# Performance work log

Hardware: AMD Instinct MI355X
Metric: run time of the kernel (lower is better)

The kernel has to match this reference:

```python
import jax, jax.numpy as jnp
import numpy as np

N_EXPERTS = 8
TOP_K = 2
HIDDEN = 768
INTER = 2048

def setup_inputs() -> dict:
    key = jax.random.key(0)
    ks = jax.random.split(key, 12)
    s_in = 1.0 / np.sqrt(HIDDEN)
    s_mid = 1.0 / np.sqrt(INTER)
    return {
        "x": jax.random.normal(ks[0], (4, 64, 64, HIDDEN), dtype=jnp.float32),
        # gate: nn.Parameter(randn(E, d))
        "gate_w": jax.random.normal(ks[1], (N_EXPERTS, HIDDEN), dtype=jnp.float32),
        # routed experts, stacked: fc1 (d->f), fc2 (f->d)
        "fc1_w": jax.random.uniform(ks[2], (N_EXPERTS, INTER, HIDDEN), jnp.float32, -s_in, s_in),
        "fc1_b": jax.random.uniform(ks[3], (N_EXPERTS, INTER), jnp.float32, -s_in, s_in),
        "fc2_w": jax.random.uniform(ks[4], (N_EXPERTS, HIDDEN, INTER), jnp.float32, -s_mid, s_mid),
        "fc2_b": jax.random.uniform(ks[5], (N_EXPERTS, HIDDEN), jnp.float32, -s_mid, s_mid),
        # shared MLP (gated): w1 (d->f), w3 (d->f), w2 (f->d)
        "w1_w": jax.random.uniform(ks[6], (INTER, HIDDEN), jnp.float32, -s_in, s_in),
        "w1_b": jax.random.uniform(ks[7], (INTER,), jnp.float32, -s_in, s_in),
        "w3_w": jax.random.uniform(ks[8], (INTER, HIDDEN), jnp.float32, -s_in, s_in),
        "w3_b": jax.random.uniform(ks[9], (INTER,), jnp.float32, -s_in, s_in),
        "w2_w": jax.random.uniform(ks[10], (HIDDEN, INTER), jnp.float32, -s_mid, s_mid),
        "w2_b": jax.random.uniform(ks[11], (HIDDEN,), jnp.float32, -s_mid, s_mid),
    }

def _gelu(h):
    # torch nn.GELU / F.gelu default = exact (erf) form
    return jax.nn.gelu(h, approximate=False)

def reference(x, gate_w, fc1_w, fc1_b, fc2_w, fc2_b,
              w1_w, w1_b, w3_w, w3_b, w2_w, w2_b):
    B, H, W, C = x.shape
    xf = x.reshape(-1, C)                                  # [T, d]
    # gate: softmax over experts, top-k, renormalize
    scores = jax.nn.softmax(xf @ gate_w.T, axis=-1)        # [T, E]
    top_v, top_i = jax.lax.top_k(scores, TOP_K)            # [T, k]
    top_v = top_v / jnp.sum(top_v, axis=-1, keepdims=True)
    # routed experts: dense-mask combine (weight 0 => zero contribution,
    # same math as gather-GEMM-scatter without data-dependent shapes)
    out = jnp.zeros_like(xf)
    for e in range(N_EXPERTS):
        w_e = jnp.sum(jnp.where(top_i == e, top_v, 0.0), axis=-1)   # [T]
        h = _gelu(xf @ fc1_w[e].T + fc1_b[e])                        # [T, f]
        y = h @ fc2_w[e].T + fc2_b[e]                                # [T, d]
        out = out + w_e[:, None] * y
    # shared gated MLP
    shared = (_gelu(xf @ w1_w.T + w1_b) * (xf @ w3_w.T + w3_b)) @ w2_w.T + w2_b
    return (out + shared).reshape(B, H, W, C)
```

## Files before the change

### kernel.cpp

```cpp
#include <hip/hip_runtime.h>
#include <math.h>

#define T_TOK 16384
#define DH 768
#define DF 2048
#define NE 8
#define NSLOT (2 * T_TOK)
#define MT_ROUTED 264
#define NROW_H (MT_ROUTED * 128)

typedef __attribute__((ext_vector_type(8))) short bf16x8;
typedef __attribute__((ext_vector_type(4))) float f32x4;

__device__ __forceinline__ unsigned short f2bf(float f) {
  union { float f; unsigned int u; } v; v.f = f;
  unsigned int u = v.u;
  u += 0x7fffu + ((u >> 16) & 1u);
  return (unsigned short)(u >> 16);
}
__device__ __forceinline__ float bf2f(unsigned short s) {
  union { unsigned int u; float f; } v; v.u = ((unsigned int)s) << 16; return v.f;
}

__device__ __forceinline__ float gelu_exact(float x) {
  return 0.5f * x * (1.0f + erff(x * 0.70710678118654752440f));
}

__device__ __forceinline__ unsigned short* yrow(unsigned short* ylo,
                                                unsigned short* yhi, int s) {
  return (s < T_TOK) ? (ylo + (long)s * DH) : (yhi + (long)(s - T_TOK) * DH);
}

__device__ __forceinline__ void async_cp16(void* lds, const void* g) {
  __builtin_amdgcn_global_load_lds(
      (const __attribute__((address_space(1))) unsigned int*)(unsigned long long)g,
      (__attribute__((address_space(3))) unsigned int*)(unsigned int)(unsigned long long)lds,
      16, 0, 0);
}

__global__ __launch_bounds__(256) void conv_f32_bf16(
    const float* __restrict__ src, unsigned short* __restrict__ dst, int n4) {
  int i = blockIdx.x * blockDim.x + threadIdx.x;
  if (i >= n4) return;
  const float4 v = ((const float4*)src)[i];
  union { unsigned short us[4]; unsigned long long u64; } o;
  o.us[0] = f2bf(v.x); o.us[1] = f2bf(v.y); o.us[2] = f2bf(v.z); o.us[3] = f2bf(v.w);
  ((unsigned long long*)dst)[i] = o.u64;
}

__global__ __launch_bounds__(256) void gate_topk(
    const float* __restrict__ x, const float* __restrict__ gw,
    unsigned short* __restrict__ xb, int* __restrict__ eids,
    float* __restrict__ wts) {
  const int wave = threadIdx.x >> 6;
  const int lane = threadIdx.x & 63;
  const int t = blockIdx.x * 4 + wave;
  float4 xv[3];
#pragma unroll
  for (int i = 0; i < 3; ++i) {
    const int c = i * 256 + lane * 4;
    xv[i] = *(const float4*)&x[(long)t * DH + c];
    ushort4 o;
    o.x = f2bf(xv[i].x); o.y = f2bf(xv[i].y);
    o.z = f2bf(xv[i].z); o.w = f2bf(xv[i].w);
    *(ushort4*)&xb[(long)t * DH + c] = o;
  }
  float s[NE];
#pragma unroll
  for (int e = 0; e < NE; ++e) {
    float a = 0.f;
#pragma unroll
    for (int i = 0; i < 3; ++i) {
      const float4 g = *(const float4*)&gw[e * DH + i * 256 + lane * 4];
      a += xv[i].x * g.x + xv[i].y * g.y + xv[i].z * g.z + xv[i].w * g.w;
    }
    s[e] = a;
  }
#pragma unroll
  for (int off = 32; off >= 1; off >>= 1) {
#pragma unroll
    for (int e = 0; e < NE; ++e) s[e] += __shfl_xor(s[e], off);
  }
  if (lane == 0) {
    float b1 = s[0]; int i1 = 0;
#pragma unroll
    for (int e = 1; e < NE; ++e) { if (s[e] > b1) { b1 = s[e]; i1 = e; } }
    float b2 = -3.4e38f; int i2 = 0;
#pragma unroll
    for (int e = 0; e < NE; ++e) {
      if (e != i1 && s[e] > b2) { b2 = s[e]; i2 = e; }
    }
    const float ex = expf(b2 - b1);
    eids[2 * t]     = i1; wts[2 * t]     = 1.f / (1.f + ex);
    eids[2 * t + 1] = i2; wts[2 * t + 1] = ex / (1.f + ex);
  }
}

__global__ __launch_bounds__(256) void hist_k(
    const int* __restrict__ eids, int* __restrict__ hcur) {
  const int j = blockIdx.x * 256 + threadIdx.x;
  const int lane = threadIdx.x & 63;
  const int eid = eids[j];
#pragma unroll
  for (int e = 0; e < NE; ++e) {
    const unsigned long long m = __ballot(eid == e);
    const int tot = __popcll(m);
    if (tot && lane == (__ffsll((long long)m) - 1)) atomicAdd(&hcur[e * 64], tot);
  }
}

__global__ void scan_k(const int* __restrict__ hcur, int* __restrict__ sched,
                       int* __restrict__ cur2) {
  if (threadIdx.x == 0) {
    int b = 0;
#pragma unroll
    for (int e = 0; e < NE; ++e) {
      const int c = hcur[e * 64];
      sched[e] = b; sched[9 + e] = c; cur2[e * 64] = b;
      b += (c + 127) & ~127;
    }
    sched[8] = b;
  }
}

__global__ __launch_bounds__(256) void scatter_k(
    const int* __restrict__ eids, const float* __restrict__ wts,
    int* __restrict__ cur2, int* __restrict__ slot_tok,
    float* __restrict__ slot_wt, int* __restrict__ slot_pos) {
  const int j = blockIdx.x * 256 + threadIdx.x;
  const int lane = threadIdx.x & 63;
  const int eid = eids[j];
  const float w = wts[j];
#pragma unroll
  for (int e = 0; e < NE; ++e) {
    const unsigned long long m = __ballot(eid == e);
    const int tot = __popcll(m);
    if (!tot) continue;
    const int leader = __ffsll((long long)m) - 1;
    int b = 0;
    if (lane == leader) b = atomicAdd(&cur2[e * 64], tot);
    b = __shfl(b, leader);
    if (eid == e) {
      const int pos = b + __popcll(m & ((1ull << lane) - 1));
      slot_tok[pos] = j;
      slot_wt[pos] = w;
      slot_pos[j] = pos;
    }
  }
}

template <int MODE, int GX, int GTOT>
__global__ __launch_bounds__(256, 2) void gemm_k(
    const unsigned short* __restrict__ A, const unsigned short* __restrict__ B1,
    const unsigned short* __restrict__ B2, const float* __restrict__ bias1,
    const float* __restrict__ bias2, float* __restrict__ outF,
    unsigned short* __restrict__ outH, int K,
    const int* __restrict__ sched, const int* __restrict__ slot_tok,
    const int* __restrict__ slot_pos, const float* __restrict__ wts,
    unsigned short* __restrict__ ylo, unsigned short* __restrict__ yhi) {
  constexpr int BPX = (GTOT + 7) / 8;
  const int id = blockIdx.x;
  const int yx = (id & 7) * BPX + (id >> 3);
  const int n0 = (yx % GX) * 128;
  const int m0 = (yx / GX) * 128;

  const int tid = threadIdx.x;
  const int wave = tid >> 6;
  const int lane = tid & 63;
  const int wm = wave >> 1, wn = wave & 1;
  const int l16 = lane & 15, quad = lane >> 4;

  const unsigned short* Bbase = B1;
  const float* bias = bias1;
  int cnt_end = 0;
  if constexpr (MODE == 1 || MODE == 3 || MODE == 4) {
    if (m0 >= sched[8]) return;
    int e = 0;
#pragma unroll
    for (int i = 1; i < NE; ++i) { if (m0 >= sched[i]) e = i; }
    cnt_end = sched[e] + sched[9 + e];
    Bbase = B1 + (long)e * ((long)DF * DH);
    bias = bias1 + e * ((MODE == 1) ? DF : DH);
  }

  __shared__ __align__(16) unsigned short As[128 * 32];
  __shared__ __align__(16) unsigned short Bs[128 * 32];
  __shared__ __align__(16) unsigned short Cs[(MODE == 0) ? 128 * 32 : 16];

  const int srow0 = wave * 16 + (lane >> 2);
  const int srow1 = 64 + srow0;
  const int scol = (lane & 3) * 8;

  long ar0, ar1;
  if constexpr (MODE == 1) {
    const int p0 = m0 + srow0, p1 = m0 + srow1;
    const int t0 = (p0 < cnt_end) ? (slot_tok[p0] >> 1) : 0;
    const int t1 = (p1 < cnt_end) ? (slot_tok[p1] >> 1) : 0;
    ar0 = (long)t0 * K; ar1 = (long)t1 * K;
  } else {
    ar0 = (long)(m0 + srow0) * K;
    ar1 = (long)(m0 + srow1) * K;
  }
  const unsigned short* ap0 = A + ar0 + scol;
  const unsigned short* ap1 = A + ar1 + scol;
  const unsigned short* bp0 = Bbase + (long)(n0 + srow0) * K + scol;
  const unsigned short* bp1 = Bbase + (long)(n0 + srow1) * K + scol;
  const unsigned short* cp0 = nullptr; const unsigned short* cp1 = nullptr;
  if constexpr (MODE == 0) {
    cp0 = B2 + (long)(n0 + srow0) * K + scol;
    cp1 = B2 + (long)(n0 + srow1) * K + scol;
  }

  unsigned short* AsW = &As[wave * 512];
  unsigned short* BsW = &Bs[wave * 512];
  unsigned short* CsW = nullptr;
  if constexpr (MODE == 0) CsW = &Cs[wave * 512];

  f32x4 acc[4][4];
  f32x4 acc2[(MODE == 0) ? 4 : 1][(MODE == 0) ? 4 : 1];
#pragma unroll
  for (int i = 0; i < 4; ++i) {
#pragma unroll
    for (int j = 0; j < 4; ++j) {
      acc[i][j] = {0.f, 0.f, 0.f, 0.f};
      if constexpr (MODE == 0) acc2[i][j] = {0.f, 0.f, 0.f, 0.f};
    }
  }

  const int KT = K >> 5;
  for (int kt = 0; kt < KT; ++kt) {
    const int ko = kt << 5;
    async_cp16(AsW,        ap0 + ko);
    async_cp16(AsW + 2048, ap1 + ko);
    async_cp16(BsW,        bp0 + ko);
    async_cp16(BsW + 2048, bp1 + ko);
    if constexpr (MODE == 0) {
      async_cp16(CsW,        cp0 + ko);
      async_cp16(CsW + 2048, cp1 + ko);
    }
    __syncthreads();

    bf16x8 af[4], bfr[4], cfr[(MODE == 0) ? 4 : 1];
#pragma unroll
    for (int mi = 0; mi < 4; ++mi)
      af[mi] = *(const bf16x8*)&As[(wm * 64 + mi * 16 + l16) * 32 + quad * 8];
#pragma unroll
    for (int ni = 0; ni < 4; ++ni) {
      bfr[ni] = *(const bf16x8*)&Bs[(wn * 64 + ni * 16 + l16) * 32 + quad * 8];
      if constexpr (MODE == 0)
        cfr[ni] = *(const bf16x8*)&Cs[(wn * 64 + ni * 16 + l16) * 32 + quad * 8];
    }
#pragma unroll
    for (int mi = 0; mi < 4; ++mi) {
#pragma unroll
      for (int ni = 0; ni < 4; ++ni) {
        acc[mi][ni] = __builtin_amdgcn_mfma_f32_16x16x32_bf16(
            af[mi], bfr[ni], acc[mi][ni], 0, 0, 0);
        if constexpr (MODE == 0)
          acc2[mi][ni] = __builtin_amdgcn_mfma_f32_16x16x32_bf16(
              af[mi], cfr[ni], acc2[mi][ni], 0, 0, 0);
      }
    }
    __syncthreads();
  }

#pragma unroll
  for (int mi = 0; mi < 4; ++mi) {
#pragma unroll
    for (int r = 0; r < 4; ++r) {
      const int row = m0 + wm * 64 + mi * 16 + quad * 4 + r;
      if constexpr (MODE == 3) {
        unsigned short* yr = yrow(ylo, yhi, row);
#pragma unroll
        for (int ni = 0; ni < 4; ++ni) {
          const int c = n0 + wn * 64 + ni * 16 + l16;
          yr[c] = f2bf(acc[mi][ni][r] + bias[c]);
        }
      } else if constexpr (MODE == 4) {
        if (row < cnt_end) {
          const int t = slot_tok[row] >> 1;
          const float w = wts[row];
#pragma unroll
          for (int ni = 0; ni < 4; ++ni) {
            const int c = n0 + wn * 64 + ni * 16 + l16;
            atomicAdd(&outF[(long)t * DH + c], w * (acc[mi][ni][r] + bias[c]));
          }
        }
      } else if constexpr (MODE == 2) {
        const int s0 = slot_pos[2 * row], s1 = slot_pos[2 * row + 1];
        const float w0 = wts[2 * row], w1 = wts[2 * row + 1];
        const unsigned short* y0 = yrow(ylo, yhi, s0);
        const unsigned short* y1 = yrow(ylo, yhi, s1);
#pragma unroll
        for (int ni = 0; ni < 4; ++ni) {
          const int c = n0 + wn * 64 + ni * 16 + l16;
          outF[(long)row * DH + c] =
              acc[mi][ni][r] + bias[c] + w0 * bf2f(y0[c]) + w1 * bf2f(y1[c]);
        }
      } else if constexpr (MODE == 5) {
#pragma unroll
        for (int ni = 0; ni < 4; ++ni) {
          const int c = n0 + wn * 64 + ni * 16 + l16;
          outF[(long)row * DH + c] = acc[mi][ni][r] + bias[c];
        }
      } else if constexpr (MODE == 1) {
#pragma unroll
        for (int ni = 0; ni < 4; ++ni) {
          const int c = n0 + wn * 64 + ni * 16 + l16;
          outH[(long)row * DF + c] = f2bf(gelu_exact(acc[mi][ni][r] + bias[c]));
        }
      } else {
#pragma unroll
        for (int ni = 0; ni < 4; ++ni) {
          const int c = n0 + wn * 64 + ni * 16 + l16;
          const float h1 = acc[mi][ni][r] + bias[c];
          const float h3 = acc2[mi][ni][r] + bias2[c];
          outH[(long)row * DF + c] = f2bf(gelu_exact(h1) * h3);
        }
      }
    }
  }
}

extern "C" void kernel_launch(void* const* d_in, const int* in_sizes, int n_in,
                              void* d_out, int out_size, void* d_ws, size_t ws_size,
                              hipStream_t stream) {
  const float* x     = (const float*)d_in[0];
  const float* gw    = (const float*)d_in[1];
  const float* fc1w  = (const float*)d_in[2];
  const float* fc1bs = (const float*)d_in[3];
  const float* fc2w  = (const float*)d_in[4];
  const float* fc2bs = (const float*)d_in[5];
  const float* w1w   = (const float*)d_in[6];
  const float* w1bs  = (const float*)d_in[7];
  const float* w3w   = (const float*)d_in[8];
  const float* w3bs  = (const float*)d_in[9];
  const float* w2w   = (const float*)d_in[10];
  const float* w2bs  = (const float*)d_in[11];
  float* out = (float*)d_out;

  char* p = (char*)d_ws;
  auto take = [&](size_t b) { char* r = p; p += (b + 255) & ~(size_t)255; return r; };
  unsigned short* xb   = (unsigned short*)take((size_t)T_TOK * DH * 2);
  unsigned short* fc1b = (unsigned short*)take((size_t)NE * DF * DH * 2);
  unsigned short* fc2b = (unsigned short*)take((size_t)NE * DH * DF * 2);
  unsigned short* w1b  = (unsigned short*)take((size_t)DF * DH * 2);
  unsigned short* w3b  = (unsigned short*)take((size_t)DF * DH * 2);
  unsigned short* w2b  = (unsigned short*)take((size_t)DH * DF * 2);
  unsigned short* h    = (unsigned short*)take((size_t)NROW_H * DF * 2);
  int*   eids     = (int*)take((size_t)NSLOT * 4);
  float* wts      = (float*)take((size_t)NSLOT * 4);
  int*   hcur     = (int*)take(NE * 64 * 4);
  int*   cur2     = (int*)take(NE * 64 * 4);
  int*   sched    = (int*)take(32 * 4);
  int*   slot_tok = (int*)take((size_t)NROW_H * 4);
  float* slot_wt  = (float*)take((size_t)NROW_H * 4);
  int*   slot_pos = (int*)take((size_t)NSLOT * 4);

  const size_t yhi_bytes = (size_t)(NROW_H - T_TOK) * DH * 2;
  const bool pathA = ((size_t)(p - (char*)d_ws) + yhi_bytes) <= ws_size;
  unsigned short* ylo = fc1b;
  unsigned short* yhi = pathA ? (unsigned short*)take(yhi_bytes) : nullptr;

  hipMemsetAsync(hcur, 0, NE * 64 * sizeof(int), stream);

  auto conv = [&](const float* s, unsigned short* d, long n) {
    int n4 = (int)(n >> 2);
    conv_f32_bf16<<<(n4 + 255) / 256, 256, 0, stream>>>(s, d, n4);
  };
  conv(fc1w, fc1b, (long)NE * DF * DH);
  conv(fc2w, fc2b, (long)NE * DH * DF);
  conv(w1w, w1b, (long)DF * DH);
  conv(w3w, w3b, (long)DF * DH);
  conv(w2w, w2b, (long)DH * DF);

  gate_topk<<<T_TOK / 4, 256, 0, stream>>>(x, gw, xb, eids, wts);
  hist_k<<<NSLOT / 256, 256, 0, stream>>>(eids, hcur);
  scan_k<<<1, 64, 0, stream>>>(hcur, sched, cur2);
  scatter_k<<<NSLOT / 256, 256, 0, stream>>>(eids, wts, cur2, slot_tok, slot_wt,
                                             slot_pos);

  if (pathA) {
    gemm_k<1, 16, 16 * MT_ROUTED><<<16 * MT_ROUTED, 256, 0, stream>>>(
        xb, fc1b, nullptr, fc1bs, nullptr, nullptr, h, DH,
        sched, slot_tok, nullptr, nullptr, nullptr, nullptr);
    gemm_k<3, 6, 6 * MT_ROUTED><<<6 * MT_ROUTED, 256, 0, stream>>>(
        h, fc2b, nullptr, fc2bs, nullptr, nullptr, nullptr, DF,
        sched, nullptr, nullptr, nullptr, ylo, yhi);
    gemm_k<0, 16, 16 * (T_TOK / 128)><<<16 * (T_TOK / 128), 256, 0, stream>>>(
        xb, w1b, w3b, w1bs, w3bs, nullptr, h, DH,
        nullptr, nullptr, nullptr, nullptr, nullptr, nullptr);
    gemm_k<2, 6, 6 * (T_TOK / 128)><<<6 * (T_TOK / 128), 256, 0, stream>>>(
        h, w2b, nullptr, w2bs, nullptr, out, nullptr, DF,
        nullptr, nullptr, slot_pos, wts, ylo, yhi);
  } else {
    gemm_k<0, 16, 16 * (T_TOK / 128)><<<16 * (T_TOK / 128), 256, 0, stream>>>(
        xb, w1b, w3b, w1bs, w3bs, nullptr, h, DH,
        nullptr, nullptr, nullptr, nullptr, nullptr, nullptr);
    gemm_k<5, 6, 6 * (T_TOK / 128)><<<6 * (T_TOK / 128), 256, 0, stream>>>(
        h, w2b, nullptr, w2bs, nullptr, out, nullptr, DF,
        nullptr, nullptr, nullptr, nullptr, nullptr, nullptr);
    gemm_k<1, 16, 16 * MT_ROUTED><<<16 * MT_ROUTED, 256, 0, stream>>>(
        xb, fc1b, nullptr, fc1bs, nullptr, nullptr, h, DH,
        sched, slot_tok, nullptr, nullptr, nullptr, nullptr);
    gemm_k<4, 6, 6 * MT_ROUTED><<<6 * MT_ROUTED, 256, 0, stream>>>(
        h, fc2b, nullptr, fc2bs, nullptr, out, nullptr, DF,
        sched, slot_tok, nullptr, slot_wt, nullptr, nullptr);
  }
}
```

Before: 745.0 us.

## Replace 128x128 GEMM with 256x256 double-buffered 8-wave MFMA kernel

Replaces the single-buffered 128x128, 4-wave GEMM with a 256x256 tile, 512-thread kernel. The new kernel double-buffers its 128KB LDS tiles and uses 64-wide K steps, XOR-swizzled LDS layout, explicit waitcnt/barrier scheduling and s_setprio around MFMA bursts. The shared gated MLP now interleaves the w1 and w3 rows into one weight matrix, so a single B operand yields both gate and up outputs. Expert padding grows to 256 rows. The aim is more reuse per tile and overlap of global loads with MFMA, at the cost of fewer blocks, more padding waste, and very high register/LDS pressure that limits occupancy.

```diff
diff --git a/kernel.cpp b/kernel.cpp
--- a/kernel.cpp
+++ b/kernel.cpp
@@ -6,8 +6,9 @@
 #define DF 2048
 #define NE 8
 #define NSLOT (2 * T_TOK)
-#define MT_ROUTED 264
-#define NROW_H (MT_ROUTED * 128)
+#define MT_R 135
+#define NROW_H (MT_R * 256)
+#define YSPLIT 16384
 
 typedef __attribute__((ext_vector_type(8))) short bf16x8;
 typedef __attribute__((ext_vector_type(4))) float f32x4;
@@ -28,7 +29,7 @@
 
 __device__ __forceinline__ unsigned short* yrow(unsigned short* ylo,
                                                 unsigned short* yhi, int s) {
-  return (s < T_TOK) ? (ylo + (long)s * DH) : (yhi + (long)(s - T_TOK) * DH);
+  return (s < YSPLIT) ? (ylo + (long)s * DH) : (yhi + (long)(s - YSPLIT) * DH);
 }
 
 __device__ __forceinline__ void async_cp16(void* lds, const void* g) {
@@ -48,6 +49,20 @@
   ((unsigned long long*)dst)[i] = o.u64;
 }
 
+__global__ __launch_bounds__(192) void conv_interleave_k(
+    const float* __restrict__ w1, const float* __restrict__ w3,
+    unsigned short* __restrict__ dst) {
+  const int row = blockIdx.x;
+  const int q = row >> 5, s = row & 31;
+  const float* src = (s < 16) ? &w1[(long)(q * 16 + s) * DH]
+                              : &w3[(long)(q * 16 + (s - 16)) * DH];
+  const int c = threadIdx.x * 4;
+  const float4 v = *(const float4*)&src[c];
+  ushort4 o;
+  o.x = f2bf(v.x); o.y = f2bf(v.y); o.z = f2bf(v.z); o.w = f2bf(v.w);
+  *(ushort4*)&dst[(long)row * DH + c] = o;
+}
+
 __global__ __launch_bounds__(256) void gate_topk(
     const float* __restrict__ x, const float* __restrict__ gw,
     unsigned short* __restrict__ xb, int* __restrict__ eids,
@@ -117,7 +132,7 @@
     for (int e = 0; e < NE; ++e) {
       const int c = hcur[e * 64];
       sched[e] = b; sched[9 + e] = c; cur2[e * 64] = b;
-      b += (c + 127) & ~127;
+      b += (c + 255) & ~255;
     }
     sched[8] = b;
   }
@@ -149,25 +164,103 @@
   }
 }
 
-template <int MODE, int GX, int GTOT>
-__global__ __launch_bounds__(256, 2) void gemm_k(
+#define FENCE asm volatile("" ::: "memory")
+#define BAR { FENCE; __builtin_amdgcn_s_barrier(); FENCE; }
+#define WAIT_LGKM0 asm volatile("s_waitcnt lgkmcnt(0)" ::: "memory")
+#define WAIT_VM4 asm volatile("s_waitcnt vmcnt(4)" ::: "memory")
+#define WAIT_VM0 asm volatile("s_waitcnt vmcnt(0)" ::: "memory")
+
+#define RD_A(BUF, MI, KS) \
+  (*(const bf16x8*)(aBase + (BUF) * 32768 + (MI) * 2048 + colk[KS] * 2))
+#define RD_B(BUF, NI, KS) \
+  (*(const bf16x8*)(bBase + (BUF) * 32768 + (NI) * 2048 + colk[KS] * 2))
+
+#define STAGE_A(BUF, H, KO)                                                     \
+  {                                                                             \
+    async_cp16(smem + (BUF) * 32768 + (H) * 16384 + ldsW, apS##H##0 + (KO));    \
+    async_cp16(smem + (BUF) * 32768 + (H) * 16384 + 8192 + ldsW,                \
+               apS##H##1 + (KO));                                               \
+  }
+#define STAGE_B(BUF, H, KO)                                                     \
+  {                                                                             \
+    async_cp16(smem + 65536 + (BUF) * 32768 + (H) * 16384 + ldsW,               \
+               bpS##H##0 + (KO));                                               \
+    async_cp16(smem + 65536 + (BUF) * 32768 + (H) * 16384 + 8192 + ldsW,        \
+               bpS##H##1 + (KO));                                               \
+  }
+
+#define MFMA16(AF, BF, MB)                                                      \
+  _Pragma("unroll") for (int mi_ = 0; mi_ < 4; ++mi_) {                         \
+    _Pragma("unroll") for (int ni_ = 0; ni_ < 4; ++ni_) {                       \
+      acc[(MB) + mi_][ni_] = __builtin_amdgcn_mfma_f32_16x16x32_bf16(           \
+          AF[mi_], BF[ni_], acc[(MB) + mi_][ni_], 0, 0, 0);                     \
+    }                                                                           \
+  }
+
+#define GROUP(BUF, S0, S1, S2, S3, VMW)                                         \
+  {                                                                             \
+    bf16x8 aA[4], aB[4], aC[4], aD[4], bX[4], bY[4];                            \
+    _Pragma("unroll") for (int i = 0; i < 4; ++i) {                             \
+      aA[i] = RD_A(BUF, i, 0);                                                  \
+      bX[i] = RD_B(BUF, i, 0);                                                  \
+    }                                                                           \
+    S0;                                                                         \
+    BAR;                                                                        \
+    __builtin_amdgcn_s_setprio(1);                                              \
+    MFMA16(aA, bX, 0);                                                          \
+    __builtin_amdgcn_s_setprio(0);                                              \
+    BAR;                                                                        \
+    _Pragma("unroll") for (int i = 0; i < 4; ++i) {                             \
+      aB[i] = RD_A(BUF, 4 + i, 0);                                              \
+      aC[i] = RD_A(BUF, i, 1);                                                  \
+      aD[i] = RD_A(BUF, 4 + i, 1);                                              \
+      bY[i] = RD_B(BUF, i, 1);                                                  \
+    }                                                                           \
+    S1;                                                                         \
+    BAR;                                                                        \
+    __builtin_amdgcn_s_setprio(1);                                              \
+    MFMA16(aB, bX, 4);                                                          \
+    __builtin_amdgcn_s_setprio(0);                                              \
+    WAIT_LGKM0;                                                                 \
+    BAR;                                                                        \
+    S2;                                                                         \
+    BAR;                                                                        \
+    __builtin_amdgcn_s_setprio(1);                                              \
+    MFMA16(aC, bY, 0);                                                          \
+    __builtin_amdgcn_s_setprio(0);                                              \
+    BAR;                                                                        \
+    S3;                                                                         \
+    VMW;                                                                        \
+    BAR;                                                                        \
+    __builtin_amdgcn_s_setprio(1);                                              \
+    MFMA16(aD, bY, 4);                                                          \
+    __builtin_amdgcn_s_setprio(0);                                              \
+    BAR;                                                                        \
+  }
+
+template <int MODE, int KDIM, int GX, int GTOT>
+__global__ __launch_bounds__(512, 2) void gemm8_k(
     const unsigned short* __restrict__ A, const unsigned short* __restrict__ B1,
-    const unsigned short* __restrict__ B2, const float* __restrict__ bias1,
-    const float* __restrict__ bias2, float* __restrict__ outF,
-    unsigned short* __restrict__ outH, int K,
+    const float* __restrict__ bias1, const float* __restrict__ bias2,
+    float* __restrict__ outF, unsigned short* __restrict__ outH,
     const int* __restrict__ sched, const int* __restrict__ slot_tok,
     const int* __restrict__ slot_pos, const float* __restrict__ wts,
     unsigned short* __restrict__ ylo, unsigned short* __restrict__ yhi) {
-  constexpr int BPX = (GTOT + 7) / 8;
+  constexpr int NT = KDIM / 64;
+  constexpr int NT2 = NT / 2;
+  constexpr int Q = GTOT / 8, R = GTOT % 8;
+  static __shared__ __align__(16) char smem[131072];
+
   const int id = blockIdx.x;
-  const int yx = (id & 7) * BPX + (id >> 3);
-  const int n0 = (yx % GX) * 128;
-  const int m0 = (yx / GX) * 128;
+  const int xcd = id & 7, pos = id >> 3;
+  const int wg = (xcd < R ? xcd * (Q + 1) : R * (Q + 1) + (xcd - R) * Q) + pos;
+  const int n0 = (wg % GX) * 256;
+  const int m0 = (wg / GX) * 256;
 
   const int tid = threadIdx.x;
-  const int wave = tid >> 6;
+  const int w8 = tid >> 6;
   const int lane = tid & 63;
-  const int wm = wave >> 1, wn = wave & 1;
+  const int wm = w8 >> 2, wn = w8 & 3;
   const int l16 = lane & 15, quad = lane >> 4;
 
   const unsigned short* Bbase = B1;
@@ -183,139 +276,113 @@
     bias = bias1 + e * ((MODE == 1) ? DF : DH);
   }
 
-  __shared__ __align__(16) unsigned short As[128 * 32];
-  __shared__ __align__(16) unsigned short Bs[128 * 32];
-  __shared__ __align__(16) unsigned short Cs[(MODE == 0) ? 128 * 32 : 16];
-
-  const int srow0 = wave * 16 + (lane >> 2);
-  const int srow1 = 64 + srow0;
-  const int scol = (lane & 3) * 8;
-
-  long ar0, ar1;
-  if constexpr (MODE == 1) {
-    const int p0 = m0 + srow0, p1 = m0 + srow1;
-    const int t0 = (p0 < cnt_end) ? (slot_tok[p0] >> 1) : 0;
-    const int t1 = (p1 < cnt_end) ? (slot_tok[p1] >> 1) : 0;
-    ar0 = (long)t0 * K; ar1 = (long)t1 * K;
-  } else {
-    ar0 = (long)(m0 + srow0) * K;
-    ar1 = (long)(m0 + srow1) * K;
-  }
-  const unsigned short* ap0 = A + ar0 + scol;
-  const unsigned short* ap1 = A + ar1 + scol;
-  const unsigned short* bp0 = Bbase + (long)(n0 + srow0) * K + scol;
-  const unsigned short* bp1 = Bbase + (long)(n0 + srow1) * K + scol;
-  const unsigned short* cp0 = nullptr; const unsigned short* cp1 = nullptr;
-  if constexpr (MODE == 0) {
-    cp0 = B2 + (long)(n0 + srow0) * K + scol;
-    cp1 = B2 + (long)(n0 + srow1) * K + scol;
-  }
-
-  unsigned short* AsW = &As[wave * 512];
-  unsigned short* BsW = &Bs[wave * 512];
-  unsigned short* CsW = nullptr;
-  if constexpr (MODE == 0) CsW = &Cs[wave * 512];
-
-  f32x4 acc[4][4];
-  f32x4 acc2[(MODE == 0) ? 4 : 1][(MODE == 0) ? 4 : 1];
-#pragma unroll
-  for (int i = 0; i < 4; ++i) {
-#pragma unroll
-    for (int j = 0; j < 4; ++j) {
-      acc[i][j] = {0.f, 0.f, 0.f, 0.f};
-      if constexpr (MODE == 0) acc2[i][j] = {0.f, 0.f, 0.f, 0.f};
-    }
-  }
-
-  const int KT = K >> 5;
-  for (int kt = 0; kt < KT; ++kt) {
-    const int ko = kt << 5;
-    async_cp16(AsW,        ap0 + ko);
-    async_cp16(AsW + 2048, ap1 + ko);
-    async_cp16(BsW,        bp0 + ko);
-    async_cp16(BsW + 2048, bp1 + ko);
-    if constexpr (MODE == 0) {
-      async_cp16(CsW,        cp0 + ko);
-      async_cp16(CsW + 2048, cp1 + ko);
-    }
-    __syncthreads();
-
-    bf16x8 af[4], bfr[4], cfr[(MODE == 0) ? 4 : 1];
-#pragma unroll
-    for (int mi = 0; mi < 4; ++mi)
-      af[mi] = *(const bf16x8*)&As[(wm * 64 + mi * 16 + l16) * 32 + quad * 8];
-#pragma unroll
-    for (int ni = 0; ni < 4; ++ni) {
-      bfr[ni] = *(const bf16x8*)&Bs[(wn * 64 + ni * 16 + l16) * 32 + quad * 8];
-      if constexpr (MODE == 0)
-        cfr[ni] = *(const bf16x8*)&Cs[(wn * 64 + ni * 16 + l16) * 32 + quad * 8];
-    }
-#pragma unroll
-    for (int mi = 0; mi < 4; ++mi) {
-#pragma unroll
-      for (int ni = 0; ni < 4; ++ni) {
-        acc[mi][ni] = __builtin_amdgcn_mfma_f32_16x16x32_bf16(
-            af[mi], bfr[ni], acc[mi][ni], 0, 0, 0);
-        if constexpr (MODE == 0)
-          acc2[mi][ni] = __builtin_amdgcn_mfma_f32_16x16x32_bf16(
-              af[mi], cfr[ni], acc2[mi][ni], 0, 0, 0);
-      }
-    }
-    __syncthreads();
-  }
-
-#pragma unroll
-  for (int mi = 0; mi < 4; ++mi) {
+  const int scol = ((lane & 7) << 3) ^ ((lane & 32) >> 1);
+  auto asrc = [&](int hh, int j) -> const unsigned short* {
+    const int rr = j * 64 + w8 * 8 + (lane >> 3);
+    long arow;
+    if constexpr (MODE == 1) {
+      const int slot = m0 + hh * 128 + rr;
+      arow = (slot < cnt_end) ? (long)(slot_tok[slot] >> 1) : 0L;
+    } else {
+      arow = (long)(m0 + hh * 128 + rr);
+    }
+    return A + arow * KDIM + scol;
+  };
+  auto bsrc = [&](int hh, int j) -> const unsigned short* {
+    const int rr = j * 64 + w8 * 8 + (lane >> 3);
+    return Bbase + (long)(n0 + hh * 128 + rr) * KDIM + scol;
+  };
+  const unsigned short* apS00 = asrc(0, 0);
+  const unsigned short* apS01 = asrc(0, 1);
+  const unsigned short* apS10 = asrc(1, 0);
+  const unsigned short* apS11 = asrc(1, 1);
+  const unsigned short* bpS00 = bsrc(0, 0);
+  const unsigned short* bpS01 = bsrc(0, 1);
+  const unsigned short* bpS10 = bsrc(1, 0);
+  const unsigned short* bpS11 = bsrc(1, 1);
+  const int ldsW = w8 * 1024;
+
+  const int swz = ((l16 >> 2) & 1) << 4;
+  const int colk[2] = { (quad * 8) ^ swz, (32 + quad * 8) ^ swz };
+  const char* aBase = smem + (wm * 128 + l16) * 128;
+  const char* bBase = smem + 65536 + (wn * 64 + l16) * 128;
+
+  f32x4 acc[8][4];
+#pragma unroll
+  for (int i = 0; i < 8; ++i)
+#pragma unroll
+    for (int j = 0; j < 4; ++j) acc[i][j] = {0.f, 0.f, 0.f, 0.f};
+
+  STAGE_A(0, 0, 0) STAGE_A(0, 1, 0) STAGE_B(0, 0, 0) STAGE_B(0, 1, 0)
+  STAGE_A(1, 0, 64) STAGE_A(1, 1, 64)
+  WAIT_VM4;
+  BAR;
+
+  int ko = 0;
+#pragma unroll 1
+  for (int it = 0; it < NT2 - 1; ++it, ko += 128) {
+    GROUP(0, STAGE_B(1, 0, ko + 64), STAGE_B(1, 1, ko + 64),
+          STAGE_A(0, 0, ko + 128), STAGE_A(0, 1, ko + 128), WAIT_VM4)
+    GROUP(1, STAGE_B(0, 0, ko + 128), STAGE_B(0, 1, ko + 128),
+          STAGE_A(1, 0, ko + 192), STAGE_A(1, 1, ko + 192), WAIT_VM4)
+  }
+  GROUP(0, STAGE_B(1, 0, ko + 64), STAGE_B(1, 1, ko + 64), (void)0, (void)0,
+        WAIT_VM0)
+  GROUP(1, (void)0, (void)0, (void)0, (void)0, (void)0)
+
+  const int ccol0 = n0 + wn * 64;
+#pragma unroll
+  for (int mi = 0; mi < 8; ++mi) {
 #pragma unroll
     for (int r = 0; r < 4; ++r) {
-      const int row = m0 + wm * 64 + mi * 16 + quad * 4 + r;
-      if constexpr (MODE == 3) {
+      const int row = m0 + wm * 128 + mi * 16 + quad * 4 + r;
+      if constexpr (MODE == 1) {
+#pragma unroll
+        for (int ni = 0; ni < 4; ++ni) {
+          const int c = ccol0 + ni * 16 + l16;
+          outH[(long)row * DF + c] = f2bf(gelu_exact(acc[mi][ni][r] + bias[c]));
+        }
+      } else if constexpr (MODE == 0) {
+#pragma unroll
+        for (int p = 0; p < 2; ++p) {
+          const int ch = (n0 >> 1) + wn * 32 + p * 16 + l16;
+          const float h1 = acc[mi][2 * p][r] + bias1[ch];
+          const float h3 = acc[mi][2 * p + 1][r] + bias2[ch];
+          outH[(long)row * DF + ch] = f2bf(gelu_exact(h1) * h3);
+        }
+      } else if constexpr (MODE == 3) {
         unsigned short* yr = yrow(ylo, yhi, row);
 #pragma unroll
         for (int ni = 0; ni < 4; ++ni) {
-          const int c = n0 + wn * 64 + ni * 16 + l16;
+          const int c = ccol0 + ni * 16 + l16;
           yr[c] = f2bf(acc[mi][ni][r] + bias[c]);
         }
-      } else if constexpr (MODE == 4) {
+      } else if constexpr (MODE == 2) {
+        const int s0 = slot_pos[2 * row], s1 = slot_pos[2 * row + 1];
+        const float w0v = wts[2 * row], w1v = wts[2 * row + 1];
+        const unsigned short* y0 = yrow(ylo, yhi, s0);
+        const unsigned short* y1 = yrow(ylo, yhi, s1);
+#pragma unroll
+        for (int ni = 0; ni < 4; ++ni) {
+          const int c = ccol0 + ni * 16 + l16;
+          outF[(long)row * DH + c] =
+              acc[mi][ni][r] + bias1[c] + w0v * bf2f(y0[c]) + w1v * bf2f(y1[c]);
+        }
+      } else if constexpr (MODE == 5) {
+#pragma unroll
+        for (int ni = 0; ni < 4; ++ni) {
+          const int c = ccol0 + ni * 16 + l16;
+          outF[(long)row * DH + c] = acc[mi][ni][r] + bias1[c];
+        }
+      } else {
         if (row < cnt_end) {
           const int t = slot_tok[row] >> 1;
           const float w = wts[row];
 #pragma unroll
           for (int ni = 0; ni < 4; ++ni) {
-            const int c = n0 + wn * 64 + ni * 16 + l16;
+            const int c = ccol0 + ni * 16 + l16;
             atomicAdd(&outF[(long)t * DH + c], w * (acc[mi][ni][r] + bias[c]));
           }
-        }
-      } else if constexpr (MODE == 2) {
-        const int s0 = slot_pos[2 * row], s1 = slot_pos[2 * row + 1];
-        const float w0 = wts[2 * row], w1 = wts[2 * row + 1];
-        const unsigned short* y0 = yrow(ylo, yhi, s0);
-        const unsigned short* y1 = yrow(ylo, yhi, s1);
-#pragma unroll
-        for (int ni = 0; ni < 4; ++ni) {
-          const int c = n0 + wn * 64 + ni * 16 + l16;
-          outF[(long)row * DH + c] =
-              acc[mi][ni][r] + bias[c] + w0 * bf2f(y0[c]) + w1 * bf2f(y1[c]);
-        }
-      } else if constexpr (MODE == 5) {
-#pragma unroll
-        for (int ni = 0; ni < 4; ++ni) {
-          const int c = n0 + wn * 64 + ni * 16 + l16;
-          outF[(long)row * DH + c] = acc[mi][ni][r] + bias[c];
-        }
-      } else if constexpr (MODE == 1) {
-#pragma unroll
-        for (int ni = 0; ni < 4; ++ni) {
-          const int c = n0 + wn * 64 + ni * 16 + l16;
-          outH[(long)row * DF + c] = f2bf(gelu_exact(acc[mi][ni][r] + bias[c]));
-        }
-      } else {
-#pragma unroll
-        for (int ni = 0; ni < 4; ++ni) {
-          const int c = n0 + wn * 64 + ni * 16 + l16;
-          const float h1 = acc[mi][ni][r] + bias[c];
-          const float h3 = acc2[mi][ni][r] + bias2[c];
-          outH[(long)row * DF + c] = f2bf(gelu_exact(h1) * h3);
         }
       }
     }
@@ -344,8 +411,7 @@
   unsigned short* xb   = (unsigned short*)take((size_t)T_TOK * DH * 2);
   unsigned short* fc1b = (unsigned short*)take((size_t)NE * DF * DH * 2);
   unsigned short* fc2b = (unsigned short*)take((size_t)NE * DH * DF * 2);
-  unsigned short* w1b  = (unsigned short*)take((size_t)DF * DH * 2);
-  unsigned short* w3b  = (unsigned short*)take((size_t)DF * DH * 2);
+  unsigned short* bint = (unsigned short*)take((size_t)2 * DF * DH * 2);
   unsigned short* w2b  = (unsigned short*)take((size_t)DH * DF * 2);
   unsigned short* h    = (unsigned short*)take((size_t)NROW_H * DF * 2);
   int*   eids     = (int*)take((size_t)NSLOT * 4);
@@ -357,7 +423,7 @@
   float* slot_wt  = (float*)take((size_t)NROW_H * 4);
   int*   slot_pos = (int*)take((size_t)NSLOT * 4);
 
-  const size_t yhi_bytes = (size_t)(NROW_H - T_TOK) * DH * 2;
+  const size_t yhi_bytes = (size_t)(NROW_H - YSPLIT) * DH * 2;
   const bool pathA = ((size_t)(p - (char*)d_ws) + yhi_bytes) <= ws_size;
   unsigned short* ylo = fc1b;
   unsigned short* yhi = pathA ? (unsigned short*)take(yhi_bytes) : nullptr;
@@ -370,9 +436,8 @@
   };
   conv(fc1w, fc1b, (long)NE * DF * DH);
   conv(fc2w, fc2b, (long)NE * DH * DF);
-  conv(w1w, w1b, (long)DF * DH);
-  conv(w3w, w3b, (long)DF * DH);
   conv(w2w, w2b, (long)DH * DF);
+  conv_interleave_k<<<2 * DF, 192, 0, stream>>>(w1w, w3w, bint);
 
   gate_topk<<<T_TOK / 4, 256, 0, stream>>>(x, gw, xb, eids, wts);
   hist_k<<<NSLOT / 256, 256, 0, stream>>>(eids, hcur);
@@ -381,30 +446,30 @@
                                              slot_pos);
 
   if (pathA) {
-    gemm_k<1, 16, 16 * MT_ROUTED><<<16 * MT_ROUTED, 256, 0, stream>>>(
-        xb, fc1b, nullptr, fc1bs, nullptr, nullptr, h, DH,
+    gemm8_k<1, DH, 8, 8 * MT_R><<<8 * MT_R, 512, 0, stream>>>(
+        xb, fc1b, fc1bs, nullptr, nullptr, h,
         sched, slot_tok, nullptr, nullptr, nullptr, nullptr);
-    gemm_k<3, 6, 6 * MT_ROUTED><<<6 * MT_ROUTED, 256, 0, stream>>>(
-        h, fc2b, nullptr, fc2bs, nullptr, nullptr, nullptr, DF,
+    gemm8_k<3, DF, 3, 3 * MT_R><<<3 * MT_R, 512, 0, stream>>>(
+        h, fc2b, fc2bs, nullptr, nullptr, nullptr,
         sched, nullptr, nullptr, nullptr, ylo, yhi);
-    gemm_k<0, 16, 16 * (T_TOK / 128)><<<16 * (T_TOK / 128), 256, 0, stream>>>(
-        xb, w1b, w3b, w1bs, w3bs, nullptr, h, DH,
+    gemm8_k<0, DH, 16, 1024><<<1024, 512, 0, stream>>>(
+        xb, bint, w1bs, w3bs, nullptr, h,
         nullptr, nullptr, nullptr, nullptr, nullptr, nullptr);
-    gemm_k<2, 6, 6 * (T_TOK / 128)><<<6 * (T_TOK / 128), 256, 0, stream>>>(
-        h, w2b, nullptr, w2bs, nullptr, out, nullptr, DF,
+    gemm8_k<2, DF, 3, 192><<<192, 512, 0, stream>>>(
+        h, w2b, w2bs, nullptr, out, nullptr,
         nullptr, nullptr, slot_pos, wts, ylo, yhi);
   } else {
-    gemm_k<0, 16, 16 * (T_TOK / 128)><<<16 * (T_TOK / 128), 256, 0, stream>>>(
-        xb, w1b, w3b, w1bs, w3bs, nullptr, h, DH,
+    gemm8_k<0, DH, 16, 1024><<<1024, 512, 0, stream>>>(
+        xb, bint, w1bs, w3bs, nullptr, h,
         nullptr, nullptr, nullptr, nullptr, nullptr, nullptr);
-    gemm_k<5, 6, 6 * (T_TOK / 128)><<<6 * (T_TOK / 128), 256, 0, stream>>>(
-        h, w2b, nullptr, w2bs, nullptr, out, nullptr, DF,
+    gemm8_k<5, DF, 3, 192><<<192, 512, 0, stream>>>(
+        h, w2b, w2bs, nullptr, out, nullptr,
         nullptr, nullptr, nullptr, nullptr, nullptr, nullptr);
-    gemm_k<1, 16, 16 * MT_ROUTED><<<16 * MT_ROUTED, 256, 0, stream>>>(
-        xb, fc1b, nullptr, fc1bs, nullptr, nullptr, h, DH,
+    gemm8_k<1, DH, 8, 8 * MT_R><<<8 * MT_R, 512, 0, stream>>>(
+        xb, fc1b, fc1bs, nullptr, nullptr, h,
         sched, slot_tok, nullptr, nullptr, nullptr, nullptr);
-    gemm_k<4, 6, 6 * MT_ROUTED><<<6 * MT_ROUTED, 256, 0, stream>>>(
-        h, fc2b, nullptr, fc2bs, nullptr, out, nullptr, DF,
+    gemm8_k<4, DF, 3, 3 * MT_R><<<3 * MT_R, 512, 0, stream>>>(
+        h, fc2b, fc2bs, nullptr, out, nullptr,
         sched, slot_tok, nullptr, slot_wt, nullptr, nullptr);
   }
 }
```

Result: slower. 948.7 us (+27.3%).

## Double-buffer LDS tiles and XOR-swizzle chunks to avoid bank conflicts

Applied to the files above, without the earlier changes.

The GEMM main loop now keeps two LDS buffers per operand and issues the async global-to-LDS copies for the next K-slice before computing on the current one, so memory latency can overlap with the MFMA work. It also XOR-swizzles which 16-byte chunk each lane loads into a row, and undoes the swizzle on the fragment reads, to reduce LDS bank conflicts. The cost is twice the LDS footprint, which may lower occupancy, especially in the three-operand gated mode.

```diff
diff --git a/kernel.cpp b/kernel.cpp
--- a/kernel.cpp
+++ b/kernel.cpp
@@ -183,13 +183,14 @@
     bias = bias1 + e * ((MODE == 1) ? DF : DH);
   }
 
-  __shared__ __align__(16) unsigned short As[128 * 32];
-  __shared__ __align__(16) unsigned short Bs[128 * 32];
-  __shared__ __align__(16) unsigned short Cs[(MODE == 0) ? 128 * 32 : 16];
+  __shared__ __align__(16) unsigned short As[2][128 * 32];
+  __shared__ __align__(16) unsigned short Bs[2][128 * 32];
+  __shared__ __align__(16) unsigned short Cs[(MODE == 0) ? 2 : 1]
+                                            [(MODE == 0) ? 128 * 32 : 16];
 
   const int srow0 = wave * 16 + (lane >> 2);
   const int srow1 = 64 + srow0;
-  const int scol = (lane & 3) * 8;
+  const int scol = (((lane & 3) ^ ((lane >> 3) & 3)) << 3);
 
   long ar0, ar1;
   if constexpr (MODE == 1) {
@@ -211,10 +212,7 @@
     cp1 = B2 + (long)(n0 + srow1) * K + scol;
   }
 
-  unsigned short* AsW = &As[wave * 512];
-  unsigned short* BsW = &Bs[wave * 512];
-  unsigned short* CsW = nullptr;
-  if constexpr (MODE == 0) CsW = &Cs[wave * 512];
+  const int woff = wave * 512;
 
   f32x4 acc[4][4];
   f32x4 acc2[(MODE == 0) ? 4 : 1][(MODE == 0) ? 4 : 1];
@@ -227,28 +225,37 @@
     }
   }
 
+  auto stage = [&](int b, int kt) {
+    const int ko = kt << 5;
+    async_cp16(&As[b][woff],        ap0 + ko);
+    async_cp16(&As[b][woff + 2048], ap1 + ko);
+    async_cp16(&Bs[b][woff],        bp0 + ko);
+    async_cp16(&Bs[b][woff + 2048], bp1 + ko);
+    if constexpr (MODE == 0) {
+      async_cp16(&Cs[b][woff],        cp0 + ko);
+      async_cp16(&Cs[b][woff + 2048], cp1 + ko);
+    }
+  };
+
+  const int rchunk = ((quad ^ ((l16 >> 1) & 3)) << 3);
+
   const int KT = K >> 5;
+  stage(0, 0);
+  __syncthreads();
+
   for (int kt = 0; kt < KT; ++kt) {
-    const int ko = kt << 5;
-    async_cp16(AsW,        ap0 + ko);
-    async_cp16(AsW + 2048, ap1 + ko);
-    async_cp16(BsW,        bp0 + ko);
-    async_cp16(BsW + 2048, bp1 + ko);
-    if constexpr (MODE == 0) {
-      async_cp16(CsW,        cp0 + ko);
-      async_cp16(CsW + 2048, cp1 + ko);
-    }
-    __syncthreads();
+    const int b = kt & 1;
+    if (kt + 1 < KT) stage(b ^ 1, kt + 1);
 
     bf16x8 af[4], bfr[4], cfr[(MODE == 0) ? 4 : 1];
 #pragma unroll
     for (int mi = 0; mi < 4; ++mi)
-      af[mi] = *(const bf16x8*)&As[(wm * 64 + mi * 16 + l16) * 32 + quad * 8];
+      af[mi] = *(const bf16x8*)&As[b][(wm * 64 + mi * 16 + l16) * 32 + rchunk];
 #pragma unroll
     for (int ni = 0; ni < 4; ++ni) {
-      bfr[ni] = *(const bf16x8*)&Bs[(wn * 64 + ni * 16 + l16) * 32 + quad * 8];
+      bfr[ni] = *(const bf16x8*)&Bs[b][(wn * 64 + ni * 16 + l16) * 32 + rchunk];
       if constexpr (MODE == 0)
-        cfr[ni] = *(const bf16x8*)&Cs[(wn * 64 + ni * 16 + l16) * 32 + quad * 8];
+        cfr[ni] = *(const bf16x8*)&Cs[b][(wn * 64 + ni * 16 + l16) * 32 + rchunk];
     }
 #pragma unroll
     for (int mi = 0; mi < 4; ++mi) {
```

New measurement: 734.9 us. About the same (-1.4%).
